# Optimization experiments

Hardware: AMD Instinct MI355X
Metric: run time of the kernel (lower is better)

## Reference

```python
import jax, jax.numpy as jnp
import numpy as np

H, I, E, TOPK = 2048, 1408, 8, 2
B, S = 2, 2048


def setup_inputs() -> dict:
    key = jax.random.key(0)
    k1, k2, k3, k4, k5 = jax.random.split(key, 5)
    x = jax.random.normal(k1, (B, S, H), dtype=jnp.float32)
    expert_indices = jax.random.randint(k2, (B, S, TOPK), 0, E, dtype=jnp.int64)
    expert_weights = jax.random.uniform(k3, (B, S, TOPK), dtype=jnp.float32)
    # params: w13 = concat([gate, up], dim=1) -> [E, 2I, H]; down_proj [E, H, I]
    w13 = jax.random.normal(k4, (E, 2 * I, H), dtype=jnp.float32) * 0.02
    down_proj = jax.random.normal(k5, (E, H, I), dtype=jnp.float32) * 0.02
    return {"x": x, "expert_indices": expert_indices, "expert_weights": expert_weights,
            "w13": w13, "down_proj": down_proj}


def _moe(x, expert_indices, expert_weights, w13, down_proj):
    b, s, h = x.shape
    T = b * s
    x_flat = x.reshape(T, h)
    idx = expert_indices.reshape(T, -1)            # [T, top_k]
    wts = expert_weights.reshape(T, -1)            # [T, top_k]
    # dense combine weights: routing[t, e] = sum of weights of slots routed to e
    # (matches original scatter/index_add combine, including duplicate experts)
    routing = jnp.zeros((T, w13.shape[0]), x.dtype).at[
        jnp.arange(T)[:, None], idx].add(wts)      # [T, E]
    # per-expert SwiGLU MLP computed densely, zeroed out by routing weights
    gu = jnp.einsum('th,eih->tei', x_flat, w13)    # [T, E, 2I]
    g, u = jnp.split(gu, 2, axis=-1)
    hact = jax.nn.silu(g) * u                      # [T, E, I]
    y = jnp.einsum('tei,ehi->teh', hact, down_proj)  # [T, E, H]
    out = jnp.einsum('te,teh->th', routing, y)     # [T, H]
    return out.reshape(b, s, h)


def reference(x, expert_indices, expert_weights, w13, down_proj):
    return _moe(x, expert_indices, expert_weights, w13, down_proj)
```

## Files before the change

kernel.cpp:

```cpp
#include <hip/hip_runtime.h>
#include <hip/hip_bf16.h>


typedef __bf16 bf16;
typedef bf16 bf16x8 __attribute__((ext_vector_type(8)));
typedef float f32x4 __attribute__((ext_vector_type(4)));

constexpr int Hdim = 2048;
constexpr int Idim = 1408;
constexpr int NE = 8;
constexpr int TOPK = 2;
constexpr int NT = 4096;
constexpr int NPAIR = 8192;
constexpr int BK = 64;
constexpr int NX8 = NT * Hdim / 8;
constexpr int NW8 = NE * 2 * Idim * Hdim / 8;
constexpr int ND8 = NE * Hdim * Idim / 8;

#define GLOAD16(G, L) __builtin_amdgcn_global_load_lds(                    \
    (const __attribute__((address_space(1))) void*)(G),                    \
    (__attribute__((address_space(3))) void*)(L), 16, 0, 0)


__global__ void k_cvt3(const float* __restrict__ x, bf16* __restrict__ xb,
                       const float* __restrict__ w13, bf16* __restrict__ w13b,
                       const float* __restrict__ dp, bf16* __restrict__ dpb) {
    int i = blockIdx.x * 256 + threadIdx.x;
    const float* s;
    bf16* d;
    int off;
    if (i < NX8) { s = x; d = xb; off = i; }
    else if (i < NX8 + NW8) { s = w13; d = w13b; off = i - NX8; }
    else if (i < NX8 + NW8 + ND8) { s = dp; d = dpb; off = i - NX8 - NW8; }
    else return;
    f32x4 a = *reinterpret_cast<const f32x4*>(s + (size_t)off * 8);
    f32x4 b = *reinterpret_cast<const f32x4*>(s + (size_t)off * 8 + 4);
    bf16x8 v;
#pragma unroll
    for (int j = 0; j < 4; j++) { v[j] = (bf16)a[j]; v[4 + j] = (bf16)b[j]; }
    *reinterpret_cast<bf16x8*>(d + (size_t)off * 8) = v;
}


__global__ void k_bin1(const int* __restrict__ eidx, int* __restrict__ chunkhist) {
    __shared__ int h[NE];
    int t = threadIdx.x;
    if (t < NE) h[t] = 0;
    __syncthreads();
    int p = blockIdx.x * 256 + t;
    atomicAdd(&h[eidx[p]], 1);
    __syncthreads();
    if (t < NE) chunkhist[blockIdx.x * NE + t] = h[t];
}

__global__ void k_bin2(int* __restrict__ meta, const int* __restrict__ chunkhist,
                       int* __restrict__ chunkbase) {
    if (threadIdx.x == 0) {
        int counts[NE];
        for (int e = 0; e < NE; e++) counts[e] = 0;
        for (int b = 0; b < 32; b++)
            for (int e = 0; e < NE; e++) {
                chunkbase[b * NE + e] = counts[e];
                counts[e] += chunkhist[b * NE + e];
            }
        int acc = 0;
        for (int e = 0; e < NE; e++) {
            meta[e] = counts[e];
            meta[8 + e] = acc;
            acc += counts[e];
        }
    }
}

__global__ void k_bin3(const int* __restrict__ eidx, const float* __restrict__ wts,
                       const int* __restrict__ meta, const int* __restrict__ chunkbase,
                       int* __restrict__ token_id, float* __restrict__ weightv) {
    __shared__ int earr[256];
    int t = threadIdx.x;
    int p = blockIdx.x * 256 + t;
    int e = eidx[p];
    earr[t] = e;
    __syncthreads();
    int rank = 0;
    for (int q = 0; q < t; q++) rank += (earr[q] == e) ? 1 : 0;
    int pos = meta[8 + e] + chunkbase[blockIdx.x * NE + e] + rank;
    token_id[pos] = p / TOPK;
    weightv[pos] = wts[p];
}


__global__ __launch_bounds__(256, 2) void k_gemm1(
    const bf16* __restrict__ xb, const bf16* __restrict__ w13b,
    const int* __restrict__ meta, bf16* __restrict__ hact) {
    const int flat = blockIdx.x;
    const int work = (flat & 7) * 264 + (flat >> 3);
    const int mslot = work % 12;
    const int grp = work / 12;
    const int e = grp / 22;
    const int ytile = grp - e * 22;

    const int n_e = meta[e];
    const int m0 = mslot * 128;
    if (m0 >= n_e) return;
    const int base = meta[8 + e];
    const int* toks = (const int*)(meta + 64) + base;
    const bf16* wg = w13b + (size_t)e * (2 * Idim) * Hdim + (size_t)(ytile * 64) * Hdim;
    const bf16* wu = wg + (size_t)Idim * Hdim;

    __shared__ bf16 As[128 * 64];
    __shared__ bf16 Bg[64 * 64];
    __shared__ bf16 Bu[64 * 64];

    const int tid = threadIdx.x;
    const int lane = tid & 63;
    const int wid = tid >> 6;
    const int wr = wid >> 1, wc = wid & 1;
    const int l16 = lane & 15, lq = lane >> 4;

    const bf16* gA[4];
    const bf16* gG[2];
    const bf16* gU[2];
    int loA[4], loB[2];
#pragma unroll
    for (int r = 0; r < 4; r++) {
        int sid = r * 256 + tid;
        int row = sid >> 3, seg = sid & 7;
        int ss = seg ^ (row & 7);
        loA[r] = (r * 256 + (tid & ~63)) * 16;
        int rr = m0 + row;
        if (rr >= n_e) rr = n_e - 1;
        gA[r] = xb + (size_t)toks[rr] * Hdim + ss * 8;
    }
#pragma unroll
    for (int r = 0; r < 2; r++) {
        int sid = r * 256 + tid;
        int row = sid >> 3, seg = sid & 7;
        int ss = seg ^ (row & 7);
        loB[r] = (r * 256 + (tid & ~63)) * 16;
        gG[r] = wg + (size_t)row * Hdim + ss * 8;
        gU[r] = wu + (size_t)row * Hdim + ss * 8;
    }

    f32x4 accg[4][2], accu[4][2];
#pragma unroll
    for (int m = 0; m < 4; m++)
#pragma unroll
        for (int n = 0; n < 2; n++) {
            accg[m][n] = f32x4{0.f, 0.f, 0.f, 0.f};
            accu[m][n] = f32x4{0.f, 0.f, 0.f, 0.f};
        }

    for (int k0 = 0; k0 < Hdim; k0 += BK) {
        __syncthreads();
#pragma unroll
        for (int r = 0; r < 4; r++) GLOAD16(gA[r] + k0, (char*)As + loA[r]);
#pragma unroll
        for (int r = 0; r < 2; r++) {
            GLOAD16(gG[r] + k0, (char*)Bg + loB[r]);
            GLOAD16(gU[r] + k0, (char*)Bu + loB[r]);
        }
        __syncthreads();
#pragma unroll
        for (int kk = 0; kk < 2; ++kk) {
            bf16x8 af[4], bgf[2], buf_[2];
#pragma unroll
            for (int m = 0; m < 4; m++) {
                int row = wr * 64 + m * 16 + l16;
                int s = (kk * 4 + lq) ^ (row & 7);
                af[m] = *reinterpret_cast<const bf16x8*>(&As[row * 64 + s * 8]);
            }
#pragma unroll
            for (int n = 0; n < 2; n++) {
                int row = wc * 32 + n * 16 + l16;
                int s = (kk * 4 + lq) ^ (row & 7);
                bgf[n] = *reinterpret_cast<const bf16x8*>(&Bg[row * 64 + s * 8]);
                buf_[n] = *reinterpret_cast<const bf16x8*>(&Bu[row * 64 + s * 8]);
            }
#pragma unroll
            for (int m = 0; m < 4; m++)
#pragma unroll
                for (int n = 0; n < 2; n++) {
                    accg[m][n] = __builtin_amdgcn_mfma_f32_16x16x32_bf16(af[m], bgf[n], accg[m][n], 0, 0, 0);
                    accu[m][n] = __builtin_amdgcn_mfma_f32_16x16x32_bf16(af[m], buf_[n], accu[m][n], 0, 0, 0);
                }
        }
    }

    const int colbase = ytile * 64 + wc * 32;
#pragma unroll
    for (int m = 0; m < 4; m++) {
        int lr0 = m0 + wr * 64 + m * 16 + lq * 4;
#pragma unroll
        for (int j = 0; j < 4; j++) {
            int lr = lr0 + j;
            if (lr < n_e) {
                size_t rowoff = (size_t)(base + lr) * Idim;
#pragma unroll
                for (int n = 0; n < 2; n++) {
                    float g = accg[m][n][j], u = accu[m][n][j];
                    float v = (g / (1.f + __expf(-g))) * u;
                    hact[rowoff + colbase + n * 16 + l16] = (bf16)v;
                }
            }
        }
    }
}


__global__ __launch_bounds__(256, 2) void k_gemm2(
    const bf16* __restrict__ hact, const bf16* __restrict__ dpb,
    const int* __restrict__ meta, const float* __restrict__ weightv,
    float* __restrict__ out) {
    const int flat = blockIdx.x;
    const int work = (flat & 7) * 192 + (flat >> 3);
    const int mslot = work % 12;
    const int grp = work / 12;
    const int e = grp >> 4;
    const int ytile = grp & 15;

    const int n_e = meta[e];
    const int m0 = mslot * 128;
    if (m0 >= n_e) return;
    const int base = meta[8 + e];
    const int* toks = (const int*)(meta + 64) + base;
    const bf16* wb = dpb + (size_t)e * Hdim * Idim + (size_t)(ytile * 128) * Idim;

    __shared__ bf16 As[128 * 64];
    __shared__ bf16 Bs[128 * 64];

    const int tid = threadIdx.x;
    const int lane = tid & 63;
    const int wid = tid >> 6;
    const int wr = wid >> 1, wc = wid & 1;
    const int l16 = lane & 15, lq = lane >> 4;

    const bf16* gA[4];
    const bf16* gB[4];
    int lo[4];
#pragma unroll
    for (int r = 0; r < 4; r++) {
        int sid = r * 256 + tid;
        int row = sid >> 3, seg = sid & 7;
        int ss = seg ^ (row & 7);
        lo[r] = (r * 256 + (tid & ~63)) * 16;
        int rr = m0 + row;
        if (rr >= n_e) rr = n_e - 1;
        gA[r] = hact + (size_t)(base + rr) * Idim + ss * 8;
        gB[r] = wb + (size_t)row * Idim + ss * 8;
    }

    f32x4 acc[4][4];
#pragma unroll
    for (int m = 0; m < 4; m++)
#pragma unroll
        for (int n = 0; n < 4; n++) acc[m][n] = f32x4{0.f, 0.f, 0.f, 0.f};

    for (int k0 = 0; k0 < Idim; k0 += BK) {
        __syncthreads();
#pragma unroll
        for (int r = 0; r < 4; r++) {
            GLOAD16(gA[r] + k0, (char*)As + lo[r]);
            GLOAD16(gB[r] + k0, (char*)Bs + lo[r]);
        }
        __syncthreads();
#pragma unroll
        for (int kk = 0; kk < 2; ++kk) {
            bf16x8 af[4], bf_[4];
#pragma unroll
            for (int m = 0; m < 4; m++) {
                int row = wr * 64 + m * 16 + l16;
                int s = (kk * 4 + lq) ^ (row & 7);
                af[m] = *reinterpret_cast<const bf16x8*>(&As[row * 64 + s * 8]);
            }
#pragma unroll
            for (int n = 0; n < 4; n++) {
                int row = wc * 64 + n * 16 + l16;
                int s = (kk * 4 + lq) ^ (row & 7);
                bf_[n] = *reinterpret_cast<const bf16x8*>(&Bs[row * 64 + s * 8]);
            }
#pragma unroll
            for (int m = 0; m < 4; m++)
#pragma unroll
                for (int n = 0; n < 4; n++)
                    acc[m][n] = __builtin_amdgcn_mfma_f32_16x16x32_bf16(af[m], bf_[n], acc[m][n], 0, 0, 0);
        }
    }

    const int colbase = ytile * 128 + wc * 64;
#pragma unroll
    for (int m = 0; m < 4; m++) {
        int lr0 = m0 + wr * 64 + m * 16 + lq * 4;
#pragma unroll
        for (int j = 0; j < 4; j++) {
            int lr = lr0 + j;
            if (lr < n_e) {
                int tok = toks[lr];
                float w = weightv[base + lr];
#pragma unroll
                for (int n = 0; n < 4; n++) {
                    float v = acc[m][n][j] * w;
                    unsafeAtomicAdd(&out[(size_t)tok * Hdim + colbase + n * 16 + l16], v);
                }
            }
        }
    }
}


extern "C" void kernel_launch(void* const* d_in, const int* in_sizes, int n_in,
                              void* d_out, int out_size, void* d_ws, size_t ws_size,
                              hipStream_t stream) {
    const float* x = (const float*)d_in[0];
    const int* eidx = (const int*)d_in[1];
    const float* ewts = (const float*)d_in[2];
    const float* w13 = (const float*)d_in[3];
    const float* dproj = (const float*)d_in[4];
    float* out = (float*)d_out;

    char* ws = (char*)d_ws;
    int* meta = (int*)ws;
    int* token_id = meta + 64;
    float* weightv = (float*)(meta + 64 + NPAIR);
    int* chunkhist = meta + 64 + 2 * NPAIR;
    int* chunkbase = chunkhist + 256;
    bf16* xb = (bf16*)(ws + 67840);
    bf16* w13b = xb + (size_t)NT * Hdim;
    bf16* dpb = w13b + (size_t)NE * 2 * Idim * Hdim;
    bf16* hact = dpb + (size_t)NE * Hdim * Idim;

    hipMemsetAsync(d_out, 0, (size_t)out_size * sizeof(float), stream);

    k_cvt3<<<(NX8 + NW8 + ND8 + 255) / 256, 256, 0, stream>>>(x, xb, w13, w13b, dproj, dpb);

    k_bin1<<<32, 256, 0, stream>>>(eidx, chunkhist);
    k_bin2<<<1, 64, 0, stream>>>(meta, chunkhist, chunkbase);
    k_bin3<<<32, 256, 0, stream>>>(eidx, ewts, meta, chunkbase, token_id, weightv);

    k_gemm1<<<2112, 256, 0, stream>>>(xb, w13b, meta, hact);
    k_gemm2<<<1536, 256, 0, stream>>>(hact, dpb, meta, weightv, out);
}
```

Measured before the change: 335.3 us.

## Overlap down_proj conversion with gemm1 and fold output zeroing into prep kernel

```diff
diff --git a/kernel.cpp b/kernel.cpp
--- a/kernel.cpp
+++ b/kernel.cpp
@@ -16,29 +16,40 @@
 constexpr int NX8 = NT * Hdim / 8;
 constexpr int NW8 = NE * 2 * Idim * Hdim / 8;
 constexpr int ND8 = NE * Hdim * Idim / 8;
+constexpr int PRE_CVT_BLKS = (NX8 + NW8) / 256;
+constexpr int G1_BLKS = 2112;
+constexpr int G1D_BLKS = ND8 / 256;
 
 #define GLOAD16(G, L) __builtin_amdgcn_global_load_lds(                    \
     (const __attribute__((address_space(1))) void*)(G),                    \
     (__attribute__((address_space(3))) void*)(L), 16, 0, 0)
 
 
-__global__ void k_cvt3(const float* __restrict__ x, bf16* __restrict__ xb,
-                       const float* __restrict__ w13, bf16* __restrict__ w13b,
-                       const float* __restrict__ dp, bf16* __restrict__ dpb) {
-    int i = blockIdx.x * 256 + threadIdx.x;
-    const float* s;
-    bf16* d;
-    int off;
-    if (i < NX8) { s = x; d = xb; off = i; }
-    else if (i < NX8 + NW8) { s = w13; d = w13b; off = i - NX8; }
-    else if (i < NX8 + NW8 + ND8) { s = dp; d = dpb; off = i - NX8 - NW8; }
-    else return;
-    f32x4 a = *reinterpret_cast<const f32x4*>(s + (size_t)off * 8);
-    f32x4 b = *reinterpret_cast<const f32x4*>(s + (size_t)off * 8 + 4);
-    bf16x8 v;
-#pragma unroll
-    for (int j = 0; j < 4; j++) { v[j] = (bf16)a[j]; v[4 + j] = (bf16)b[j]; }
-    *reinterpret_cast<bf16x8*>(d + (size_t)off * 8) = v;
+__global__ void k_pre(const float* __restrict__ x, bf16* __restrict__ xb,
+                      const float* __restrict__ w13, bf16* __restrict__ w13b,
+                      float* __restrict__ out, int out_n) {
+    int b = blockIdx.x;
+    if (b < PRE_CVT_BLKS) {
+        int i = b * 256 + threadIdx.x;
+        const float* s;
+        bf16* d;
+        int off;
+        if (i < NX8) { s = x; d = xb; off = i; }
+        else { s = w13; d = w13b; off = i - NX8; }
+        f32x4 a = *reinterpret_cast<const f32x4*>(s + (size_t)off * 8);
+        f32x4 c = *reinterpret_cast<const f32x4*>(s + (size_t)off * 8 + 4);
+        bf16x8 v;
+#pragma unroll
+        for (int j = 0; j < 4; j++) { v[j] = (bf16)a[j]; v[4 + j] = (bf16)c[j]; }
+        *reinterpret_cast<bf16x8*>(d + (size_t)off * 8) = v;
+    } else {
+        int i = (b - PRE_CVT_BLKS) * 2048 + threadIdx.x * 8;
+        if (i + 8 <= out_n) {
+            f32x4 z = f32x4{0.f, 0.f, 0.f, 0.f};
+            *reinterpret_cast<f32x4*>(out + i) = z;
+            *reinterpret_cast<f32x4*>(out + i + 4) = z;
+        }
+    }
 }
 
 
@@ -91,7 +102,18 @@
 
 __global__ __launch_bounds__(256, 2) void k_gemm1(
     const bf16* __restrict__ xb, const bf16* __restrict__ w13b,
-    const int* __restrict__ meta, bf16* __restrict__ hact) {
+    const int* __restrict__ meta, bf16* __restrict__ hact,
+    const float* __restrict__ dp, bf16* __restrict__ dpb) {
+    if (blockIdx.x >= G1_BLKS) {
+        int i = (blockIdx.x - G1_BLKS) * 256 + threadIdx.x;
+        f32x4 a = *reinterpret_cast<const f32x4*>(dp + (size_t)i * 8);
+        f32x4 c = *reinterpret_cast<const f32x4*>(dp + (size_t)i * 8 + 4);
+        bf16x8 v;
+#pragma unroll
+        for (int j = 0; j < 4; j++) { v[j] = (bf16)a[j]; v[4 + j] = (bf16)c[j]; }
+        *reinterpret_cast<bf16x8*>(dpb + (size_t)i * 8) = v;
+        return;
+    }
     const int flat = blockIdx.x;
     const int work = (flat & 7) * 264 + (flat >> 3);
     const int mslot = work % 12;
@@ -328,14 +350,13 @@
     bf16* dpb = w13b + (size_t)NE * 2 * Idim * Hdim;
     bf16* hact = dpb + (size_t)NE * Hdim * Idim;
 
-    hipMemsetAsync(d_out, 0, (size_t)out_size * sizeof(float), stream);
-
-    k_cvt3<<<(NX8 + NW8 + ND8 + 255) / 256, 256, 0, stream>>>(x, xb, w13, w13b, dproj, dpb);
+    const int zero_blks = (out_size + 2047) / 2048;
+    k_pre<<<PRE_CVT_BLKS + zero_blks, 256, 0, stream>>>(x, xb, w13, w13b, out, out_size);
 
     k_bin1<<<32, 256, 0, stream>>>(eidx, chunkhist);
     k_bin2<<<1, 64, 0, stream>>>(meta, chunkhist, chunkbase);
     k_bin3<<<32, 256, 0, stream>>>(eidx, ewts, meta, chunkbase, token_id, weightv);
 
-    k_gemm1<<<2112, 256, 0, stream>>>(xb, w13b, meta, hact);
+    k_gemm1<<<G1_BLKS + G1D_BLKS, 256, 0, stream>>>(xb, w13b, meta, hact, dproj, dpb);
     k_gemm2<<<1536, 256, 0, stream>>>(hact, dpb, meta, weightv, out);
 }
```

Measured after the change: 319.4 us. 1.05x faster.
